# Performance work log

Measured on AMD Instinct MI355X. Metric: run time of the kernel, lower is better.

Reference implementation:

```python
import jax, jax.numpy as jnp
import numpy as np

HEAD_SIZE = 128
LAMBDA_INIT = 0.8
FILL = 1e-09  # the module fills masked positions with 1e-9 (not -inf); reproduce faithfully


def setup_inputs() -> dict:
    key = jax.random.key(0)
    ks = jax.random.split(key, 12)
    B, T, C = 8, 2048, 1024
    q = jax.random.normal(ks[0], (B, T, C), dtype=jnp.float32)
    k = jax.random.normal(ks[1], (B, T, C), dtype=jnp.float32)
    v = jax.random.normal(ks[2], (B, T, C), dtype=jnp.float32)
    pad_mask = jax.random.randint(ks[3], (B, T), 0, 2, dtype=jnp.int32)
    scale = 1.0 / np.sqrt(C)
    Wq = jax.random.normal(ks[4], (C, 2 * HEAD_SIZE), dtype=jnp.float32) * scale
    Wk = jax.random.normal(ks[5], (C, 2 * HEAD_SIZE), dtype=jnp.float32) * scale
    Wv = jax.random.normal(ks[6], (C, HEAD_SIZE), dtype=jnp.float32) * scale
    lq1 = jax.random.normal(ks[7], (HEAD_SIZE,), dtype=jnp.float32)
    lk1 = jax.random.normal(ks[8], (HEAD_SIZE,), dtype=jnp.float32)
    lq2 = jax.random.normal(ks[9], (HEAD_SIZE,), dtype=jnp.float32)
    lk2 = jax.random.normal(ks[10], (HEAD_SIZE,), dtype=jnp.float32)
    return {"q": q, "k": k, "v": v, "pad_mask": pad_mask,
            "Wq": Wq, "Wk": Wk, "Wv": Wv,
            "lq1": lq1, "lk1": lk1, "lq2": lq2, "lk2": lk2}


def reference(q, k, v, pad_mask, Wq, Wk, Wv, lq1, lk1, lq2, lk2):
    B, T_q, C = q.shape
    T_k = k.shape[1]
    Q = q @ Wq                      # [B, Tq, 2*hs]
    K = k @ Wk                      # [B, Tk, 2*hs]
    V = v @ Wv                      # [B, Tk, ho]
    Q1, Q2 = jnp.split(Q, 2, axis=-1)
    K1, K2 = jnp.split(K, 2, axis=-1)
    s1 = jnp.einsum("bqd,bkd->bqk", Q1, K1)
    s2 = jnp.einsum("bqd,bkd->bqk", Q2, K2)
    # causal mask: tril(ones, diagonal=1) == 0 -> fill (note diagonal=1, one lookahead)
    causal_fill = jnp.tril(jnp.ones((T_q, T_k), dtype=bool), 1) == False
    s1 = jnp.where(causal_fill[None], FILL, s1)
    s2 = jnp.where(causal_fill[None], FILL, s2)
    # pad mask broadcast over the KEY axis per query row (as in original)
    pad_fill = (pad_mask == 1)[:, :, None]  # [B, Tq, 1]
    s1 = jnp.where(pad_fill, FILL, s1)
    s2 = jnp.where(pad_fill, FILL, s2)
    scale = HEAD_SIZE ** (-0.5)
    lbd = jnp.exp(jnp.dot(lq1, lk1)) - jnp.exp(jnp.dot(lq2, lk2)) + LAMBDA_INIT
    attn = jax.nn.softmax(s1 * scale, axis=-1) - lbd * jax.nn.softmax(s2 * scale, axis=-1)
    return attn @ V                 # [B, Tq, ho]
```

## Files before the change

kernel.cpp:

```cpp
#include <hip/hip_runtime.h>
#include <math.h>


#define T_SEQ 2048
#define NB 8
#define CDIM 1024
#define HS 128

constexpr float SCALE = 0.08838834764831845f;

typedef float f32x4 __attribute__((ext_vector_type(4)));
typedef __bf16 bf16x8 __attribute__((ext_vector_type(8)));
typedef unsigned int u32;

#define MFMA16 __builtin_amdgcn_mfma_f32_16x16x32_bf16

__device__ __forceinline__ void gld16(const void* g, void* l) {
  __builtin_amdgcn_global_load_lds(
      (const __attribute__((address_space(1))) u32*)g,
      (__attribute__((address_space(3))) u32*)l, 16, 0, 0);
}

__device__ __forceinline__ void wg_barrier_lds() {
  asm volatile("s_waitcnt lgkmcnt(0)" ::: "memory");
  __builtin_amdgcn_s_barrier();
  __builtin_amdgcn_sched_barrier(0);
}

__device__ __forceinline__ bf16x8 cvt8(f32x4 lo, f32x4 hi) {
  bf16x8 r;
  r[0] = (__bf16)lo.x; r[1] = (__bf16)lo.y; r[2] = (__bf16)lo.z; r[3] = (__bf16)lo.w;
  r[4] = (__bf16)hi.x; r[5] = (__bf16)hi.y; r[6] = (__bf16)hi.z; r[7] = (__bf16)hi.w;
  return r;
}

__global__ __launch_bounds__(128) void lambda_kernel(
    const float* __restrict__ lq1, const float* __restrict__ lk1,
    const float* __restrict__ lq2, const float* __restrict__ lk2,
    float* __restrict__ lbd) {
  __shared__ float r1[128], r2[128];
  int t = threadIdx.x;
  r1[t] = lq1[t] * lk1[t];
  r2[t] = lq2[t] * lk2[t];
  __syncthreads();
  for (int s = 64; s > 0; s >>= 1) {
    if (t < s) { r1[t] += r1[t + s]; r2[t] += r2[t + s]; }
    __syncthreads();
  }
  if (t == 0) *lbd = expf(r1[0]) - expf(r2[0]) + 0.8f;
}

__global__ __launch_bounds__(256) void pack_w(
    const float* __restrict__ Wq, const float* __restrict__ Wk,
    const float* __restrict__ Wv, __bf16* __restrict__ Wp) {
  int nt = blockIdx.x;
  const float* W; int colbase, N;
  if (nt < 16)      { W = Wq; colbase = nt * 16;        N = 256; }
  else if (nt < 32) { W = Wk; colbase = (nt - 16) * 16; N = 256; }
  else              { W = Wv; colbase = (nt - 32) * 16; N = 128; }
  int tid = threadIdx.x;
#pragma unroll
  for (int i = 0; i < 8; ++i) {
    int u = tid + 256 * i;
    int ks = u >> 6, lane = u & 63;
    int l15 = lane & 15, quad = lane >> 4;
    bf16x8 pk;
#pragma unroll
    for (int j = 0; j < 8; ++j)
      pk[j] = (__bf16)W[(size_t)(ks * 32 + quad * 8 + j) * N + colbase + l15];
    *(bf16x8*)(Wp + ((size_t)(nt * 32 + ks) * 64 + lane) * 8) = pk;
  }
}

template<int NT, int NTG>
__device__ __forceinline__ void proj_body(
    const float* __restrict__ Ablk, const __bf16* __restrict__ Wp,
    __bf16* __restrict__ outp, __bf16* __restrict__ Vt,
    int rows0, char* smem) {
  float*  sA = (float*)smem;
  __bf16* sB = (__bf16*)(smem + 16384);
  const int tid = threadIdx.x;
  const int lane = tid & 63, wave = tid >> 6;
  const int l15 = lane & 15, quad = lane >> 4;
  const int arow = lane >> 3;
  const int ac16 = (lane & 7) ^ arow;

  f32x4 acc0[NT], acc1[NT];
#pragma unroll
  for (int j = 0; j < NT; ++j) {
    acc0[j] = (f32x4){0.f, 0.f, 0.f, 0.f};
    acc1[j] = (f32x4){0.f, 0.f, 0.f, 0.f};
  }

  auto stage_ks = [&](int ks, int buf) {
    const float* gA = Ablk + ks * 32;
    float* lA = sA + buf * 2048;
#pragma unroll
    for (int i = 0; i < 4; ++i) {
      int li = wave * 4 + i;
      gld16(gA + (size_t)(li * 8 + arow) * CDIM + ac16 * 4, lA + li * 256);
    }
    __bf16* lB = sB + buf * 8192;
#pragma unroll
    for (int i = 0; i < 8; ++i) {
      int ntl = wave * 8 + i;
      if (ntl < NT)
        gld16(Wp + ((size_t)((NTG + ntl) * 32 + ks) * 64 + lane) * 8,
              lB + ntl * 512);
    }
  };

  stage_ks(0, 0);
  for (int ks = 0; ks < 32; ++ks) {
    const int buf = ks & 1;
    __syncthreads();
    const float* lA = sA + buf * 2048;
    int r0 = wave * 32 + l15;
    f32x4 lo0 = *(const f32x4*)(lA + r0 * 32 + (((quad * 2)     ^ (l15 & 7)) * 4));
    f32x4 hi0 = *(const f32x4*)(lA + r0 * 32 + (((quad * 2 + 1) ^ (l15 & 7)) * 4));
    bf16x8 af0 = cvt8(lo0, hi0);
    int r1 = r0 + 16;
    f32x4 lo1 = *(const f32x4*)(lA + r1 * 32 + (((quad * 2)     ^ (l15 & 7)) * 4));
    f32x4 hi1 = *(const f32x4*)(lA + r1 * 32 + (((quad * 2 + 1) ^ (l15 & 7)) * 4));
    bf16x8 af1 = cvt8(lo1, hi1);
    if (ks < 31) stage_ks(ks + 1, buf ^ 1);
    const __bf16* lB = sB + buf * 8192;
#pragma unroll
    for (int nt = 0; nt < NT; ++nt) {
      bf16x8 bf = *(const bf16x8*)(lB + nt * 512 + lane * 8);
      acc0[nt] = MFMA16(af0, bf, acc0[nt], 0, 0, 0);
      acc1[nt] = MFMA16(af1, bf, acc1[nt], 0, 0, 0);
    }
  }

  __syncthreads();
  __bf16* tile = (__bf16*)smem;
  constexpr int N = NT * 16;
#pragma unroll
  for (int half = 0; half < (NT >> 3); ++half) {
#pragma unroll
    for (int ntl = 0; ntl < 8; ++ntl) {
      f32x4 a0 = acc0[half * 8 + ntl];
      f32x4 a1 = acc1[half * 8 + ntl];
#pragma unroll
      for (int r = 0; r < 4; ++r) {
        tile[(wave * 32 + quad * 4 + r) * 136 + ntl * 16 + l15] = (__bf16)a0[r];
        tile[(wave * 32 + 16 + quad * 4 + r) * 136 + ntl * 16 + l15] = (__bf16)a1[r];
      }
    }
    __syncthreads();
#pragma unroll
    for (int i = 0; i < 8; ++i) {
      int u = tid + 128 * i;
      int row = u >> 4, c8 = u & 15;
      bf16x8 val = *(const bf16x8*)(tile + row * 136 + c8 * 8);
      *(bf16x8*)(outp + (size_t)(rows0 + row) * N + half * 128 + c8 * 8) = val;
    }
    if constexpr (NT == 8) {
      int b = rows0 >> 11, t0 = rows0 & 2047;
#pragma unroll
      for (int i = 0; i < 8; ++i) {
        int u = tid + 128 * i;
        int tc = u & 7, c = u >> 3;
        bf16x8 pk;
#pragma unroll
        for (int j = 0; j < 8; ++j) pk[j] = tile[(tc * 8 + j) * 136 + c];
        *(bf16x8*)(Vt + ((size_t)(b * 128 + c)) * T_SEQ + t0 + tc * 8) = pk;
      }
    }
    __syncthreads();
  }
}

__global__ __launch_bounds__(128, 2) void proj_mfma(
    const float* __restrict__ qin, const float* __restrict__ kin,
    const float* __restrict__ vin, const __bf16* __restrict__ Wp,
    __bf16* __restrict__ Qo, __bf16* __restrict__ Ko,
    __bf16* __restrict__ Vo, __bf16* __restrict__ Vt) {
  __shared__ char smem[49152];
  const int blk = blockIdx.x;
  const int rows0 = (blk & 255) * 64;
  if (blk < 256)
    proj_body<16, 0>(qin + (size_t)rows0 * CDIM, Wp, Qo, nullptr, rows0, smem);
  else if (blk < 512)
    proj_body<16, 16>(kin + (size_t)rows0 * CDIM, Wp, Ko, nullptr, rows0, smem);
  else
    proj_body<8, 32>(vin + (size_t)rows0 * CDIM, Wp, Vo, Vt, rows0, smem);
}

#define VCH 64
#define VCS 32
__global__ __launch_bounds__(128) void vcsum_a(const __bf16* __restrict__ V,
                                               float* __restrict__ csum) {
  int blk = blockIdx.x; int b = blk >> 6, ch = blk & 63;
  int c = threadIdx.x;
  const __bf16* vp = V + ((size_t)b * T_SEQ + ch * VCS) * HS + c;
  float s = 0.f;
#pragma unroll 4
  for (int t = 0; t < VCS; ++t) s += (float)vp[(size_t)t * HS];
  csum[(size_t)blk * HS + c] = s;
}

__global__ __launch_bounds__(128) void vcsum_b(const __bf16* __restrict__ V,
                                               const float* __restrict__ csum,
                                               float* __restrict__ cum) {
  int blk = blockIdx.x; int b = blk >> 6, ch = blk & 63;
  int c = threadIdx.x;
  float run = 0.f;
  for (int j = 0; j < ch; ++j) run += csum[(size_t)(b * VCH + j) * HS + c];
  const __bf16* vp = V + ((size_t)b * T_SEQ + ch * VCS) * HS + c;
  float* cp = cum + ((size_t)b * (T_SEQ + 1) + ch * VCS) * HS + c;
  if (ch == 0) cp[0] = 0.f;
#pragma unroll 4
  for (int t = 0; t < VCS; ++t) {
    run += (float)vp[(size_t)t * HS];
    cp[(size_t)(t + 1) * HS] = run;
  }
}

__global__ __launch_bounds__(512, 2) void attn_mfma(
    const __bf16* __restrict__ Q, const __bf16* __restrict__ K,
    const __bf16* __restrict__ Vt, const float* __restrict__ cum,
    const int* __restrict__ pad, const float* __restrict__ lbdp,
    float* __restrict__ out) {
  __shared__ __bf16 sQ[32 * 264];
  __shared__ __bf16 sK[2][64 * 256];
  __shared__ __bf16 sP[2][2][32 * 72];
  __shared__ float zb[2][32][64];
  __shared__ float zfin[2][32];

  const int tid = threadIdx.x;
  const int lane = tid & 63, wave = tid >> 6;
  const int wm = wave >> 2, wk = wave & 3;
  const int l15 = lane & 15, quad = lane >> 4;

  const int p = blockIdx.x;
  const int b = p & 7;
  const int ti = 63 - (p >> 3);
  const int q0 = ti * 32;
  const float lbd = *lbdp;
  const __bf16* Qb = Q + (size_t)b * T_SEQ * 256;
  const __bf16* Kb = K + (size_t)b * T_SEQ * 256;
  const __bf16* Vtb = Vt + (size_t)b * HS * T_SEQ;
  const float* cumb = cum + (size_t)b * (T_SEQ + 1) * HS;
  const float pc = (1.f - lbd) * (1.f / (float)T_SEQ);

  const int lastkey = q0 + 32;
  const int nkt = (min(lastkey, T_SEQ - 1) >> 6) + 1;

  auto stageK = [&](int k0, int sbuf) {
#pragma unroll
    for (int i = 0; i < 4; ++i) {
      int u = i * 512 + tid;
      int row = u >> 5, c = u & 31;
      int cg = (c & 24) | ((c ^ row) & 7);
      gld16(Kb + (size_t)(k0 + row) * 256 + cg * 8,
            &sK[sbuf][(size_t)(i * 512 + wave * 64) * 8]);
    }
  };

  stageK(0, 0);
#pragma unroll
  for (int i = 0; i < 2; ++i) {
    int c = tid + 512 * i;
    int row = c >> 5, c16 = c & 31;
    *(f32x4*)(&sQ[row * 264 + c16 * 8]) =
        *(const f32x4*)(Qb + (size_t)(q0 + row) * 256 + c16 * 8);
  }
  __syncthreads();

  bf16x8 qf[2][4];
  {
    const int row = wm * 16 + l15;
#pragma unroll
    for (int pl = 0; pl < 2; ++pl)
#pragma unroll
      for (int s = 0; s < 4; ++s)
        qf[pl][s] = *(const bf16x8*)(&sQ[row * 264 + pl * 128 + s * 32 + quad * 8]);
  }

  f32x4 O[2][2];
#pragma unroll
  for (int i = 0; i < 2; ++i)
#pragma unroll
    for (int j = 0; j < 2; ++j) O[i][j] = (f32x4){0.f, 0.f, 0.f, 0.f};
  float z[2][4] = {};

  const int kr = wk * 16 + l15;

  for (int kt = 0; kt < nkt; ++kt) {
    const int k0 = kt << 6;
    const int buf = kt & 1;
    const bool needmask = (k0 + 63 > q0 + 1);

    bf16x8 vf[2][2];
#pragma unroll
    for (int nt = 0; nt < 2; ++nt)
#pragma unroll
      for (int ks = 0; ks < 2; ++ks)
        vf[nt][ks] = *(const bf16x8*)(Vtb + (size_t)(wk * 32 + nt * 16 + l15) * T_SEQ +
                                      k0 + ks * 32 + quad * 8);
    if (kt + 1 < nkt) stageK(k0 + 64, buf ^ 1);

    f32x4 S[2];
#pragma unroll
    for (int mat = 0; mat < 2; ++mat) {
      S[mat] = (f32x4){0.f, 0.f, 0.f, 0.f};
#pragma unroll
      for (int s = 0; s < 4; ++s) {
        int cd = mat * 16 + s * 4 + quad;
        int slot = (cd & 24) | ((cd ^ kr) & 7);
        bf16x8 kfrag = *(const bf16x8*)(&sK[buf][(size_t)kr * 256 + slot * 8]);
        S[mat] = MFMA16(qf[mat][s], kfrag, S[mat], 0, 0, 0);
      }
    }

    const int rowl = wm * 16 + quad * 4;
    const int keyg = k0 + kr;
#pragma unroll
    for (int mat = 0; mat < 2; ++mat)
#pragma unroll
      for (int r = 0; r < 4; ++r) {
        float pv;
        if (needmask) {
          int rowg = q0 + rowl + r;
          pv = (keyg <= rowg + 1) ? __expf(S[mat][r] * SCALE) : 0.f;
        } else {
          pv = __expf(S[mat][r] * SCALE);
        }
        z[mat][r] += pv;
        sP[buf][mat][(rowl + r) * 72 + kr] = (__bf16)pv;
      }
    wg_barrier_lds();

#pragma unroll
    for (int ks = 0; ks < 2; ++ks) {
      bf16x8 pf0 = *(const bf16x8*)(&sP[buf][0][(wm * 16 + l15) * 72 + ks * 32 + quad * 8]);
      bf16x8 pf1 = *(const bf16x8*)(&sP[buf][1][(wm * 16 + l15) * 72 + ks * 32 + quad * 8]);
#pragma unroll
      for (int nt = 0; nt < 2; ++nt) {
        O[0][nt] = MFMA16(pf0, vf[nt][ks], O[0][nt], 0, 0, 0);
        O[1][nt] = MFMA16(pf1, vf[nt][ks], O[1][nt], 0, 0, 0);
      }
    }
    __syncthreads();
  }

#pragma unroll
  for (int mat = 0; mat < 2; ++mat)
#pragma unroll
    for (int r = 0; r < 4; ++r)
      zb[mat][wm * 16 + quad * 4 + r][wk * 16 + l15] = z[mat][r];
  __syncthreads();
  if (tid < 64) {
    int mat = tid >> 5, row = tid & 31;
    float s = 0.f;
#pragma unroll
    for (int j = 0; j < 64; ++j) s += zb[mat][row][(j + tid) & 63];
    zfin[mat][row] = s;
  }
  __syncthreads();

#pragma unroll
  for (int r = 0; r < 4; ++r) {
    const int rowl = wm * 16 + quad * 4 + r;
    const int rowg = q0 + rowl;
    const int nallow = min(rowg + 2, T_SEQ);
    const float nmask = (float)(T_SEQ - nallow);
    const float Z1 = zfin[0][rowl] + nmask;
    const float Z2 = zfin[1][rowl] + nmask;
    const float i1 = 1.f / Z1, i2 = lbd / Z2;
    const float tc = i1 - i2;
    const bool isp = (pad[b * T_SEQ + rowg] == 1);
#pragma unroll
    for (int nt = 0; nt < 2; ++nt) {
      const int col = wk * 32 + nt * 16 + l15;
      const float ct = cumb[(size_t)T_SEQ * HS + col];
      const float cn = cumb[(size_t)nallow * HS + col];
      float val = isp ? (pc * ct)
                      : (O[0][nt][r] * i1 - O[1][nt][r] * i2 + tc * (ct - cn));
      out[((size_t)b * T_SEQ + rowg) * HS + col] = val;
    }
  }
}

extern "C" void kernel_launch(void* const* d_in, const int* in_sizes, int n_in,
                              void* d_out, int out_size, void* d_ws, size_t ws_size,
                              hipStream_t stream) {
  (void)in_sizes; (void)n_in; (void)out_size; (void)ws_size;
  const float* q   = (const float*)d_in[0];
  const float* k   = (const float*)d_in[1];
  const float* v   = (const float*)d_in[2];
  const int*   pm  = (const int*)d_in[3];
  const float* Wq  = (const float*)d_in[4];
  const float* Wk  = (const float*)d_in[5];
  const float* Wv  = (const float*)d_in[6];
  const float* lq1 = (const float*)d_in[7];
  const float* lk1 = (const float*)d_in[8];
  const float* lq2 = (const float*)d_in[9];
  const float* lk2 = (const float*)d_in[10];
  float* out = (float*)d_out;
  char* ws = (char*)d_ws;

  float*  lbd  = (float*)ws;
  __bf16* Wp   = (__bf16*)(ws + 16);
  __bf16* Qp   = (__bf16*)(ws + 16 + 1310720);
  __bf16* Kp   = Qp + (size_t)NB * T_SEQ * 256;
  __bf16* Vp   = Kp + (size_t)NB * T_SEQ * 256;
  __bf16* Vt   = Vp + (size_t)NB * T_SEQ * HS;
  float*  cum  = (float*)(Vt + (size_t)NB * T_SEQ * HS);
  float*  csum = cum + (size_t)NB * (T_SEQ + 1) * HS;

  lambda_kernel<<<dim3(1), dim3(128), 0, stream>>>(lq1, lk1, lq2, lk2, lbd);
  pack_w<<<dim3(40), dim3(256), 0, stream>>>(Wq, Wk, Wv, Wp);
  proj_mfma<<<dim3(768), dim3(128), 0, stream>>>(q, k, v, Wp, Qp, Kp, Vp, Vt);
  vcsum_a<<<dim3(512), dim3(128), 0, stream>>>(Vp, csum);
  vcsum_b<<<dim3(512), dim3(128), 0, stream>>>(Vp, csum, cum);
  attn_mfma<<<dim3(512), dim3(512), 0, stream>>>(Qp, Kp, Vt, cum, pm, lbd, out);
}
```

Measured before the change: 326.5 us.

## Split projection tile across four waves in a 2x2 grid

The projection GEMM block goes from 128 to 256 threads. Waves are arranged 2x2 over rows and column tiles, so each wave holds half as many accumulators. The epilogue now writes the full output tile in one pass instead of two halves, and launch bounds rise to 3 blocks per CU. This is meant to raise occupancy and cut per-wave register pressure. In exchange, each wave reloads the A fragment and the LDS traffic per MFMA goes up.

```diff
diff --git a/kernel.cpp b/kernel.cpp
--- a/kernel.cpp
+++ b/kernel.cpp
@@ -77,17 +77,19 @@
     const float* __restrict__ Ablk, const __bf16* __restrict__ Wp,
     __bf16* __restrict__ outp, __bf16* __restrict__ Vt,
     int rows0, char* smem) {
+  constexpr int NT2 = NT / 2;
   float*  sA = (float*)smem;
   __bf16* sB = (__bf16*)(smem + 16384);
   const int tid = threadIdx.x;
   const int lane = tid & 63, wave = tid >> 6;
+  const int wr = wave >> 1, wc = wave & 1;
   const int l15 = lane & 15, quad = lane >> 4;
   const int arow = lane >> 3;
   const int ac16 = (lane & 7) ^ arow;
 
-  f32x4 acc0[NT], acc1[NT];
-#pragma unroll
-  for (int j = 0; j < NT; ++j) {
+  f32x4 acc0[NT2], acc1[NT2];
+#pragma unroll
+  for (int j = 0; j < NT2; ++j) {
     acc0[j] = (f32x4){0.f, 0.f, 0.f, 0.f};
     acc1[j] = (f32x4){0.f, 0.f, 0.f, 0.f};
   }
@@ -96,14 +98,14 @@
     const float* gA = Ablk + ks * 32;
     float* lA = sA + buf * 2048;
 #pragma unroll
+    for (int i = 0; i < 2; ++i) {
+      int li = wave * 2 + i;
+      gld16(gA + (size_t)(li * 8 + arow) * CDIM + ac16 * 4, lA + li * 256);
+    }
+    __bf16* lB = sB + buf * 8192;
+#pragma unroll
     for (int i = 0; i < 4; ++i) {
-      int li = wave * 4 + i;
-      gld16(gA + (size_t)(li * 8 + arow) * CDIM + ac16 * 4, lA + li * 256);
-    }
-    __bf16* lB = sB + buf * 8192;
-#pragma unroll
-    for (int i = 0; i < 8; ++i) {
-      int ntl = wave * 8 + i;
+      int ntl = i * 4 + wave;
       if (ntl < NT)
         gld16(Wp + ((size_t)((NTG + ntl) * 32 + ks) * 64 + lane) * 8,
               lB + ntl * 512);
@@ -115,7 +117,7 @@
     const int buf = ks & 1;
     __syncthreads();
     const float* lA = sA + buf * 2048;
-    int r0 = wave * 32 + l15;
+    int r0 = wr * 32 + l15;
     f32x4 lo0 = *(const f32x4*)(lA + r0 * 32 + (((quad * 2)     ^ (l15 & 7)) * 4));
     f32x4 hi0 = *(const f32x4*)(lA + r0 * 32 + (((quad * 2 + 1) ^ (l15 & 7)) * 4));
     bf16x8 af0 = cvt8(lo0, hi0);
@@ -126,53 +128,51 @@
     if (ks < 31) stage_ks(ks + 1, buf ^ 1);
     const __bf16* lB = sB + buf * 8192;
 #pragma unroll
-    for (int nt = 0; nt < NT; ++nt) {
-      bf16x8 bf = *(const bf16x8*)(lB + nt * 512 + lane * 8);
+    for (int nt = 0; nt < NT2; ++nt) {
+      bf16x8 bf = *(const bf16x8*)(lB + (wc * NT2 + nt) * 512 + lane * 8);
       acc0[nt] = MFMA16(af0, bf, acc0[nt], 0, 0, 0);
       acc1[nt] = MFMA16(af1, bf, acc1[nt], 0, 0, 0);
     }
   }
 
   __syncthreads();
+  constexpr int N = NT * 16;
+  constexpr int TS = N + 8;
   __bf16* tile = (__bf16*)smem;
-  constexpr int N = NT * 16;
-#pragma unroll
-  for (int half = 0; half < (NT >> 3); ++half) {
-#pragma unroll
-    for (int ntl = 0; ntl < 8; ++ntl) {
-      f32x4 a0 = acc0[half * 8 + ntl];
-      f32x4 a1 = acc1[half * 8 + ntl];
-#pragma unroll
-      for (int r = 0; r < 4; ++r) {
-        tile[(wave * 32 + quad * 4 + r) * 136 + ntl * 16 + l15] = (__bf16)a0[r];
-        tile[(wave * 32 + 16 + quad * 4 + r) * 136 + ntl * 16 + l15] = (__bf16)a1[r];
-      }
-    }
-    __syncthreads();
-#pragma unroll
-    for (int i = 0; i < 8; ++i) {
-      int u = tid + 128 * i;
-      int row = u >> 4, c8 = u & 15;
-      bf16x8 val = *(const bf16x8*)(tile + row * 136 + c8 * 8);
-      *(bf16x8*)(outp + (size_t)(rows0 + row) * N + half * 128 + c8 * 8) = val;
-    }
-    if constexpr (NT == 8) {
-      int b = rows0 >> 11, t0 = rows0 & 2047;
-#pragma unroll
-      for (int i = 0; i < 8; ++i) {
-        int u = tid + 128 * i;
-        int tc = u & 7, c = u >> 3;
-        bf16x8 pk;
-#pragma unroll
-        for (int j = 0; j < 8; ++j) pk[j] = tile[(tc * 8 + j) * 136 + c];
-        *(bf16x8*)(Vt + ((size_t)(b * 128 + c)) * T_SEQ + t0 + tc * 8) = pk;
-      }
-    }
-    __syncthreads();
-  }
-}
-
-__global__ __launch_bounds__(128, 2) void proj_mfma(
+#pragma unroll
+  for (int ntl = 0; ntl < NT2; ++ntl) {
+    f32x4 a0 = acc0[ntl];
+    f32x4 a1 = acc1[ntl];
+#pragma unroll
+    for (int r = 0; r < 4; ++r) {
+      tile[(wr * 32 + quad * 4 + r) * TS + (wc * NT2 + ntl) * 16 + l15] = (__bf16)a0[r];
+      tile[(wr * 32 + 16 + quad * 4 + r) * TS + (wc * NT2 + ntl) * 16 + l15] = (__bf16)a1[r];
+    }
+  }
+  __syncthreads();
+  constexpr int CPR = N / 8;
+#pragma unroll
+  for (int i = 0; i < (64 * CPR) / 256; ++i) {
+    int u = tid + 256 * i;
+    int row = u / CPR, c8 = u % CPR;
+    bf16x8 val = *(const bf16x8*)(tile + row * TS + c8 * 8);
+    *(bf16x8*)(outp + (size_t)(rows0 + row) * N + c8 * 8) = val;
+  }
+  if constexpr (NT == 8) {
+    int b = rows0 >> 11, t0 = rows0 & 2047;
+#pragma unroll
+    for (int i = 0; i < 4; ++i) {
+      int u = tid + 256 * i;
+      int tc = u & 7, c = u >> 3;
+      bf16x8 pk;
+#pragma unroll
+      for (int j = 0; j < 8; ++j) pk[j] = tile[(tc * 8 + j) * TS + c];
+      *(bf16x8*)(Vt + ((size_t)(b * 128 + c)) * T_SEQ + t0 + tc * 8) = pk;
+    }
+  }
+}
+
+__global__ __launch_bounds__(256, 3) void proj_mfma(
     const float* __restrict__ qin, const float* __restrict__ kin,
     const float* __restrict__ vin, const __bf16* __restrict__ Wp,
     __bf16* __restrict__ Qo, __bf16* __restrict__ Ko,
@@ -413,7 +413,7 @@
 
   lambda_kernel<<<dim3(1), dim3(128), 0, stream>>>(lq1, lk1, lq2, lk2, lbd);
   pack_w<<<dim3(40), dim3(256), 0, stream>>>(Wq, Wk, Wv, Wp);
-  proj_mfma<<<dim3(768), dim3(128), 0, stream>>>(q, k, v, Wp, Qp, Kp, Vp, Vt);
+  proj_mfma<<<dim3(768), dim3(256), 0, stream>>>(q, k, v, Wp, Qp, Kp, Vp, Vt);
   vcsum_a<<<dim3(512), dim3(128), 0, stream>>>(Vp, csum);
   vcsum_b<<<dim3(512), dim3(128), 0, stream>>>(Vp, csum, cum);
   attn_mfma<<<dim3(512), dim3(512), 0, stream>>>(Qp, Kp, Vt, cum, pm, lbd, out);
```

Measured after the change: 340.9 us. 1.04x slower.
